# Performance work log

Hardware: AMD Instinct MI355X
Metric: run time of the kernel (lower is better)

Reference implementation:

```python
import jax, jax.numpy as jnp
import numpy as np

S, B, D, K, E = 2048, 16, 256, 2048, 1048576  # seq_len, batch, input_dim, max_seq_len, n_edges


def setup_inputs() -> dict:
    key = jax.random.key(0)
    k1, k2, k3, k4, k5 = jax.random.split(key, 5)
    M = jax.random.normal(k1, (S, B, D), dtype=jnp.float32)
    W = jax.random.normal(k2, (K, D), dtype=jnp.float32) * (1.0 / np.sqrt(D))
    lengths = jax.random.randint(k3, (B,), 1, S, dtype=jnp.int64)
    edge_batch = jax.random.randint(k4, (E,), 0, B, dtype=jnp.int64)
    edge_ij = jax.random.randint(k5, (E, 2), 0, K, dtype=jnp.int64)
    return {"M": M, "W": W, "lengths": lengths, "edge_batch": edge_batch, "edge_ij": edge_ij}


def reference(M, W, lengths, edge_batch, edge_ij):
    # scale = Linear(input_dim, max_seq_len, bias=False): (S, B, K)
    scale = jnp.einsum('sbd,kd->sbk', M, W)
    # softmax over the sequence dim (dim=0), then permute(1,2,0) -> (B, K, S)
    alpha = jnp.transpose(jax.nn.softmax(scale, axis=0), (1, 2, 0))
    # mask = ones*1e-10 with edges set to 1; mask_copy = zeros with edges set to 1
    mask = jnp.full(alpha.shape, 1e-10, dtype=alpha.dtype)
    mask = mask.at[edge_batch, edge_ij[:, 0], edge_ij[:, 1]].set(1.0)
    mask_copy = jnp.zeros(alpha.shape, dtype=alpha.dtype)
    mask_copy = mask_copy.at[edge_batch, edge_ij[:, 0], edge_ij[:, 1]].set(1.0)
    masked_alpha = alpha * mask
    sums = masked_alpha.sum(-1, keepdims=True)
    scores = (masked_alpha / sums) * mask_copy
    return scores
```

## Files before the change

kernel.cpp:

```cpp
#include <hip/hip_runtime.h>

#define S_LEN 2048
#define B_DIM 16
#define D_DIM 256
#define K_DIM 2048
#define E_NUM 1048576

typedef __attribute__((ext_vector_type(4))) float f32x4;
typedef __attribute__((ext_vector_type(8))) short s16x8;
typedef __attribute__((ext_vector_type(4))) unsigned short u16x4;

__device__ __forceinline__ unsigned short f2bf(float f) {
    unsigned int u = __float_as_uint(f);
    u += 0x7fffu + ((u >> 16) & 1u);
    return (unsigned short)(u >> 16);
}

__global__ void prep_kernel(const float* __restrict__ W, const float* __restrict__ M,
                            unsigned short* __restrict__ Wbf, unsigned short* __restrict__ Mbf,
                            unsigned long long* __restrict__ mw) {
    int bid = blockIdx.x;
    if (bid < 2048) {
        int t = bid * 256 + threadIdx.x;
        ((f32x4*)mw)[t] = (f32x4){0.f, 0.f, 0.f, 0.f};
    } else if (bid < 2560) {
        int t = (bid - 2048) * 256 + threadIdx.x;
        f32x4 v = ((const f32x4*)W)[t];
        u16x4 u;
        u.x = f2bf(v.x); u.y = f2bf(v.y); u.z = f2bf(v.z); u.w = f2bf(v.w);
        ((u16x4*)Wbf)[t] = u;
    } else {
        int t = (bid - 2560) * 256 + threadIdx.x;
        f32x4 v = ((const f32x4*)M)[t];
        int flat4 = t * 4;
        int d0 = flat4 & 255;
        int sb = flat4 >> 8;
        int b  = sb & 15;
        int s  = sb >> 4;
        u16x4 u;
        u.x = f2bf(v.x); u.y = f2bf(v.y); u.z = f2bf(v.z); u.w = f2bf(v.w);
        *(u16x4*)&Mbf[((size_t)(b * S_LEN + s)) * D_DIM + d0] = u;
    }
}

__global__ void maskbuild_kernel(const int* __restrict__ eb, const int* __restrict__ ij,
                                 unsigned long long* __restrict__ mw) {
    int e = blockIdx.x * 256 + threadIdx.x;
    int b = eb[e];
    int2 p = *(const int2*)&ij[2 * e];
    size_t w = ((size_t)(b * K_DIM + p.x)) * 32 + (p.y >> 6);
    atomicOr(&mw[w], 1ull << (p.y & 63));
}

__launch_bounds__(256, 2)
__global__ void gemm6_kernel(const unsigned short* __restrict__ Mbf,
                             const unsigned short* __restrict__ Wbf,
                             const unsigned long long* __restrict__ mw,
                             float* __restrict__ out) {
    __shared__ unsigned short Msh[64 * 256];
    __shared__ float sc[64 * 128];
    __shared__ float smZ[4][2][16];
    __shared__ float smE[4][2][16];

    const int tid  = threadIdx.x;
    const int x    = blockIdx.x;
    const int b    = ((x & 7) << 1) | ((x >> 3) & 1);
    const int k0   = (x >> 4) * 64;
    const int lane = tid & 63;
    const int w    = tid >> 6;
    const int wk   = w & 1;
    const int ws   = w >> 1;
    const int r    = lane & 15;
    const int g    = lane >> 4;

    const unsigned short* MB = Mbf + (size_t)b * S_LEN * D_DIM;
    const int kc0 = k0 + wk * 32 + r;
    const size_t mrow0 = (size_t)(b * K_DIM + kc0) * 32;

    s16x8 breg[2][8];
    #pragma unroll
    for (int ks = 0; ks < 2; ++ks)
        #pragma unroll
        for (int d = 0; d < 8; ++d)
            breg[ks][d] = *(const s16x8*)&Wbf[(size_t)(kc0 + ks * 16) * D_DIM + d * 32 + g * 8];

    const int lrh  = lane >> 5;
    const int lc16 = lane & 31;

    auto stage = [&](int bufi, int t) {
        const int s0 = t * 64;
        unsigned short* buf = bufi ? (unsigned short*)sc : Msh;
        #pragma unroll
        for (int c = 0; c < 8; ++c) {
            const int row   = w * 16 + c * 2 + lrh;
            const int col16 = lc16 ^ (row & 7);
            const unsigned short* src = MB + (size_t)(s0 + row) * D_DIM + col16 * 8;
            char* dst = (char*)buf + w * 8192 + c * 1024;
            __builtin_amdgcn_global_load_lds(
                (__attribute__((address_space(1))) const void*)src,
                (__attribute__((address_space(3))) void*)dst, 16, 0, 0);
        }
    };

    float Zl[2]  = {0.f, 0.f};
    float Zel[2] = {0.f, 0.f};

    stage(0, 0);
    __syncthreads();

    for (int t = 0; t < 32; ++t) {
        if (t < 31) stage((t & 1) ^ 1, t + 1);
        const unsigned long long wv0 = mw[mrow0 + t];
        const unsigned long long wv1 = mw[mrow0 + 512 + t];
        const unsigned short* cur = (t & 1) ? (const unsigned short*)sc : Msh;

        f32x4 acc[2][2];
        #pragma unroll
        for (int q = 0; q < 2; ++q)
            #pragma unroll
            for (int ks = 0; ks < 2; ++ks) acc[q][ks] = (f32x4){0.f, 0.f, 0.f, 0.f};

        #pragma unroll
        for (int d = 0; d < 8; ++d) {
            const int acol = ((d * 4 + g) ^ (r & 7)) * 8;
            #pragma unroll
            for (int q = 0; q < 2; ++q) {
                s16x8 a = *(const s16x8*)&cur[(ws * 32 + q * 16 + r) * 256 + acol];
                acc[q][0] = __builtin_amdgcn_mfma_f32_16x16x32_bf16(a, breg[0][d], acc[q][0], 0, 0, 0);
                acc[q][1] = __builtin_amdgcn_mfma_f32_16x16x32_bf16(a, breg[1][d], acc[q][1], 0, 0, 0);
            }
        }

        #pragma unroll
        for (int q = 0; q < 2; ++q) {
            const int sh = ws * 32 + q * 16 + g * 4;
            #pragma unroll
            for (int rr = 0; rr < 4; ++rr) {
                float e0 = __expf(acc[q][0][rr]);
                float e1 = __expf(acc[q][1][rr]);
                Zl[0] += e0; Zl[1] += e1;
                Zel[0] += ((wv0 >> (sh + rr)) & 1ull) ? e0 : 0.f;
                Zel[1] += ((wv1 >> (sh + rr)) & 1ull) ? e1 : 0.f;
            }
        }
        __syncthreads();
    }

    stage(0, 0);

    #pragma unroll
    for (int ks = 0; ks < 2; ++ks) {
        Zl[ks]  += __shfl_xor(Zl[ks], 16);  Zl[ks]  += __shfl_xor(Zl[ks], 32);
        Zel[ks] += __shfl_xor(Zel[ks], 16); Zel[ks] += __shfl_xor(Zel[ks], 32);
    }
    if (g == 0) {
        smZ[w][0][r] = Zl[0]; smZ[w][1][r] = Zl[1];
        smE[w][0][r] = Zel[0]; smE[w][1][r] = Zel[1];
    }
    __syncthreads();
    float rdv[2];
    #pragma unroll
    for (int ks = 0; ks < 2; ++ks) {
        float Z  = Zl[ks]  + smZ[w ^ 2][ks][r];
        float Ze = Zel[ks] + smE[w ^ 2][ks][r];
        rdv[ks] = 1.0f / (1e-10f * (Z - Ze) + Ze);
    }

    for (int t = 0; t < 32; ++t) {
        const int h = t & 1;
        const unsigned long long wv0 = mw[mrow0 + t];
        const unsigned long long wv1 = mw[mrow0 + 512 + t];

        f32x4 acc[2][2];
        #pragma unroll
        for (int q = 0; q < 2; ++q)
            #pragma unroll
            for (int ks = 0; ks < 2; ++ks) acc[q][ks] = (f32x4){0.f, 0.f, 0.f, 0.f};

        #pragma unroll
        for (int d = 0; d < 8; ++d) {
            const int acol = ((d * 4 + g) ^ (r & 7)) * 8;
            #pragma unroll
            for (int q = 0; q < 2; ++q) {
                s16x8 a = *(const s16x8*)&Msh[(ws * 32 + q * 16 + r) * 256 + acol];
                acc[q][0] = __builtin_amdgcn_mfma_f32_16x16x32_bf16(a, breg[0][d], acc[q][0], 0, 0, 0);
                acc[q][1] = __builtin_amdgcn_mfma_f32_16x16x32_bf16(a, breg[1][d], acc[q][1], 0, 0, 0);
            }
        }

        #pragma unroll
        for (int q = 0; q < 2; ++q) {
            const int sh = ws * 32 + q * 16 + g * 4;
            #pragma unroll
            for (int ks = 0; ks < 2; ++ks) {
                const unsigned long long bits = ks ? wv1 : wv0;
                const int row = wk * 32 + ks * 16 + r;
                const int colb = h * 64 + ws * 32 + q * 16 + g * 4;
                const int phys = ((colb >> 2) ^ (row & 31));
                f32x4 v;
                #pragma unroll
                for (int rr = 0; rr < 4; ++rr) {
                    bool edge = (bits >> (sh + rr)) & 1ull;
                    v[rr] = edge ? __expf(acc[q][ks][rr]) * rdv[ks] : 0.f;
                }
                *(f32x4*)&sc[row * 128 + phys * 4] = v;
            }
        }
        __syncthreads();

        if (t < 31) stage(0, t + 1);
        if (h) {
            const int sg = t >> 1;
            const int slot = lane & 31;
            #pragma unroll
            for (int i = 0; i < 8; ++i) {
                const int row = w * 16 + i * 2 + lrh;
                f32x4 v = *(const f32x4*)&sc[row * 128 + (slot ^ (row & 31)) * 4];
                *(f32x4*)&out[(size_t)(b * K_DIM + k0 + row) * S_LEN + sg * 128 + slot * 4] = v;
            }
        }
        if (t < 31) __syncthreads();
    }
}

extern "C" void kernel_launch(void* const* d_in, const int* in_sizes, int n_in,
                              void* d_out, int out_size, void* d_ws, size_t ws_size,
                              hipStream_t stream) {
    (void)in_sizes; (void)n_in; (void)ws_size; (void)out_size;
    const float* M  = (const float*)d_in[0];
    const float* W  = (const float*)d_in[1];
    const int* eb   = (const int*)d_in[3];
    const int* ij   = (const int*)d_in[4];
    float* out      = (float*)d_out;
    char* ws        = (char*)d_ws;

    unsigned long long* mw = (unsigned long long*)ws;
    unsigned short* Wbf = (unsigned short*)(ws + 8388608);
    unsigned short* Mbf = (unsigned short*)(ws + 9437184);

    prep_kernel<<<10752, 256, 0, stream>>>(W, M, Wbf, Mbf, mw);
    maskbuild_kernel<<<E_NUM / 256, 256, 0, stream>>>(eb, ij, mw);
    gemm6_kernel<<<512, 256, 0, stream>>>(Mbf, Wbf, mw, out);
}
```

Measured before the change: 176.4 us.

## Store raw masked logits in first pass and fix up edges sparsely

Removes the second GEMM pass that recomputed the logits. The first pass now writes masked raw logits (zero off-edge) directly to the output with nontemporal stores. After the row normalisers are reduced, a sparse sweep over the edge bitmask reads back only the edge entries and overwrites them with exp(x)*rdv. This halves the MFMA work and drops the LDS transpose buffer, at the cost of scattered read-modify-write traffic on about 3% of the output and dense stores that are no longer staged through LDS.

```diff
diff --git a/kernel.cpp b/kernel.cpp
--- a/kernel.cpp
+++ b/kernel.cpp
@@ -53,14 +53,14 @@
 }
 
 __launch_bounds__(256, 2)
-__global__ void gemm6_kernel(const unsigned short* __restrict__ Mbf,
+__global__ void gemm7_kernel(const unsigned short* __restrict__ Mbf,
                              const unsigned short* __restrict__ Wbf,
                              const unsigned long long* __restrict__ mw,
                              float* __restrict__ out) {
-    __shared__ unsigned short Msh[64 * 256];
-    __shared__ float sc[64 * 128];
+    __shared__ unsigned short Msh[2][64 * 256];
     __shared__ float smZ[4][2][16];
     __shared__ float smE[4][2][16];
+    __shared__ float sm_rd[64];
 
     const int tid  = threadIdx.x;
     const int x    = blockIdx.x;
@@ -89,7 +89,7 @@
 
     auto stage = [&](int bufi, int t) {
         const int s0 = t * 64;
-        unsigned short* buf = bufi ? (unsigned short*)sc : Msh;
+        unsigned short* buf = &Msh[bufi][0];
         #pragma unroll
         for (int c = 0; c < 8; ++c) {
             const int row   = w * 16 + c * 2 + lrh;
@@ -112,7 +112,7 @@
         if (t < 31) stage((t & 1) ^ 1, t + 1);
         const unsigned long long wv0 = mw[mrow0 + t];
         const unsigned long long wv1 = mw[mrow0 + 512 + t];
-        const unsigned short* cur = (t & 1) ? (const unsigned short*)sc : Msh;
+        const unsigned short* cur = &Msh[t & 1][0];
 
         f32x4 acc[2][2];
         #pragma unroll
@@ -135,18 +135,25 @@
         for (int q = 0; q < 2; ++q) {
             const int sh = ws * 32 + q * 16 + g * 4;
             #pragma unroll
-            for (int rr = 0; rr < 4; ++rr) {
-                float e0 = __expf(acc[q][0][rr]);
-                float e1 = __expf(acc[q][1][rr]);
-                Zl[0] += e0; Zl[1] += e1;
-                Zel[0] += ((wv0 >> (sh + rr)) & 1ull) ? e0 : 0.f;
-                Zel[1] += ((wv1 >> (sh + rr)) & 1ull) ? e1 : 0.f;
+            for (int ks = 0; ks < 2; ++ks) {
+                const unsigned long long bits = ks ? wv1 : wv0;
+                f32x4 ov;
+                #pragma unroll
+                for (int rr = 0; rr < 4; ++rr) {
+                    float v = acc[q][ks][rr];
+                    float e = __expf(v);
+                    Zl[ks] += e;
+                    bool edge = (bits >> (sh + rr)) & 1ull;
+                    Zel[ks] += edge ? e : 0.f;
+                    ov[rr] = edge ? v : 0.f;
+                }
+                __builtin_nontemporal_store(ov,
+                    (f32x4*)&out[(size_t)(b * K_DIM + kc0 + ks * 16) * S_LEN
+                                 + t * 64 + ws * 32 + q * 16 + g * 4]);
             }
         }
         __syncthreads();
     }
-
-    stage(0, 0);
 
     #pragma unroll
     for (int ks = 0; ks < 2; ++ks) {
@@ -158,68 +165,29 @@
         smE[w][0][r] = Zel[0]; smE[w][1][r] = Zel[1];
     }
     __syncthreads();
-    float rdv[2];
     #pragma unroll
     for (int ks = 0; ks < 2; ++ks) {
         float Z  = Zl[ks]  + smZ[w ^ 2][ks][r];
         float Ze = Zel[ks] + smE[w ^ 2][ks][r];
-        rdv[ks] = 1.0f / (1e-10f * (Z - Ze) + Ze);
-    }
-
-    for (int t = 0; t < 32; ++t) {
-        const int h = t & 1;
-        const unsigned long long wv0 = mw[mrow0 + t];
-        const unsigned long long wv1 = mw[mrow0 + 512 + t];
-
-        f32x4 acc[2][2];
-        #pragma unroll
-        for (int q = 0; q < 2; ++q)
-            #pragma unroll
-            for (int ks = 0; ks < 2; ++ks) acc[q][ks] = (f32x4){0.f, 0.f, 0.f, 0.f};
-
-        #pragma unroll
-        for (int d = 0; d < 8; ++d) {
-            const int acol = ((d * 4 + g) ^ (r & 7)) * 8;
-            #pragma unroll
-            for (int q = 0; q < 2; ++q) {
-                s16x8 a = *(const s16x8*)&Msh[(ws * 32 + q * 16 + r) * 256 + acol];
-                acc[q][0] = __builtin_amdgcn_mfma_f32_16x16x32_bf16(a, breg[0][d], acc[q][0], 0, 0, 0);
-                acc[q][1] = __builtin_amdgcn_mfma_f32_16x16x32_bf16(a, breg[1][d], acc[q][1], 0, 0, 0);
-            }
-        }
-
-        #pragma unroll
-        for (int q = 0; q < 2; ++q) {
-            const int sh = ws * 32 + q * 16 + g * 4;
-            #pragma unroll
-            for (int ks = 0; ks < 2; ++ks) {
-                const unsigned long long bits = ks ? wv1 : wv0;
-                const int row = wk * 32 + ks * 16 + r;
-                const int colb = h * 64 + ws * 32 + q * 16 + g * 4;
-                const int phys = ((colb >> 2) ^ (row & 31));
-                f32x4 v;
-                #pragma unroll
-                for (int rr = 0; rr < 4; ++rr) {
-                    bool edge = (bits >> (sh + rr)) & 1ull;
-                    v[rr] = edge ? __expf(acc[q][ks][rr]) * rdv[ks] : 0.f;
-                }
-                *(f32x4*)&sc[row * 128 + phys * 4] = v;
-            }
-        }
-        __syncthreads();
-
-        if (t < 31) stage(0, t + 1);
-        if (h) {
-            const int sg = t >> 1;
-            const int slot = lane & 31;
-            #pragma unroll
-            for (int i = 0; i < 8; ++i) {
-                const int row = w * 16 + i * 2 + lrh;
-                f32x4 v = *(const f32x4*)&sc[row * 128 + (slot ^ (row & 31)) * 4];
-                *(f32x4*)&out[(size_t)(b * K_DIM + k0 + row) * S_LEN + sg * 128 + slot * 4] = v;
-            }
-        }
-        if (t < 31) __syncthreads();
+        float rdv = 1.0f / (1e-10f * (Z - Ze) + Ze);
+        if (ws == 0 && g == 0) sm_rd[wk * 32 + ks * 16 + r] = rdv;
+    }
+    __threadfence();
+    __syncthreads();
+
+    for (int it = tid; it < 64 * 32; it += 256) {
+        const int kl = it >> 5;
+        const int wj = it & 31;
+        unsigned long long bits = mw[(size_t)(b * K_DIM + k0 + kl) * 32 + wj];
+        if (!bits) continue;
+        const float rdrow = sm_rd[kl];
+        const size_t rowo = (size_t)(b * K_DIM + k0 + kl) * S_LEN + wj * 64;
+        while (bits) {
+            const int j = __builtin_ctzll(bits);
+            bits &= bits - 1;
+            const float xv = out[rowo + j];
+            out[rowo + j] = __expf(xv) * rdrow;
+        }
     }
 }
 
@@ -240,5 +208,5 @@
 
     prep_kernel<<<10752, 256, 0, stream>>>(W, M, Wbf, Mbf, mw);
     maskbuild_kernel<<<E_NUM / 256, 256, 0, stream>>>(eb, ij, mw);
-    gemm6_kernel<<<512, 256, 0, stream>>>(Mbf, Wbf, mw, out);
-}
+    gemm7_kernel<<<512, 256, 0, stream>>>(Mbf, Wbf, mw, out);
+}
```

Result: slower. 277.1 us (+57.1%).

## Replace two-pass GEMM softmax with single pass plus sparse finalize kernel

Applied to the files above, without the earlier changes.

The GEMM kernel previously ran the full bf16 MFMA product twice, once to accumulate softmax denominators and once to write normalized outputs. It now runs a single pass that writes raw logits at edge positions (zeros elsewhere), accumulates the sums, and stores per-row reciprocals to a workspace buffer. A new finalize kernel walks the mask bitmap and rewrites only the edge entries as exp(logit)*reciprocal. This halves the matmul work in exchange for an extra launch and a scattered read-modify-write of about a million output elements.

```diff
diff --git a/kernel.cpp b/kernel.cpp
--- a/kernel.cpp
+++ b/kernel.cpp
@@ -53,9 +53,10 @@
 }
 
 __launch_bounds__(256, 2)
-__global__ void gemm6_kernel(const unsigned short* __restrict__ Mbf,
+__global__ void gemm9_kernel(const unsigned short* __restrict__ Mbf,
                              const unsigned short* __restrict__ Wbf,
                              const unsigned long long* __restrict__ mw,
+                             float* __restrict__ rd,
                              float* __restrict__ out) {
     __shared__ unsigned short Msh[64 * 256];
     __shared__ float sc[64 * 128];
@@ -87,15 +88,14 @@
     const int lrh  = lane >> 5;
     const int lc16 = lane & 31;
 
-    auto stage = [&](int bufi, int t) {
+    auto stage = [&](int t) {
         const int s0 = t * 64;
-        unsigned short* buf = bufi ? (unsigned short*)sc : Msh;
         #pragma unroll
         for (int c = 0; c < 8; ++c) {
             const int row   = w * 16 + c * 2 + lrh;
             const int col16 = lc16 ^ (row & 7);
             const unsigned short* src = MB + (size_t)(s0 + row) * D_DIM + col16 * 8;
-            char* dst = (char*)buf + w * 8192 + c * 1024;
+            char* dst = (char*)Msh + w * 8192 + c * 1024;
             __builtin_amdgcn_global_load_lds(
                 (__attribute__((address_space(1))) const void*)src,
                 (__attribute__((address_space(3))) void*)dst, 16, 0, 0);
@@ -105,66 +105,8 @@
     float Zl[2]  = {0.f, 0.f};
     float Zel[2] = {0.f, 0.f};
 
-    stage(0, 0);
+    stage(0);
     __syncthreads();
-
-    for (int t = 0; t < 32; ++t) {
-        if (t < 31) stage((t & 1) ^ 1, t + 1);
-        const unsigned long long wv0 = mw[mrow0 + t];
-        const unsigned long long wv1 = mw[mrow0 + 512 + t];
-        const unsigned short* cur = (t & 1) ? (const unsigned short*)sc : Msh;
-
-        f32x4 acc[2][2];
-        #pragma unroll
-        for (int q = 0; q < 2; ++q)
-            #pragma unroll
-            for (int ks = 0; ks < 2; ++ks) acc[q][ks] = (f32x4){0.f, 0.f, 0.f, 0.f};
-
-        #pragma unroll
-        for (int d = 0; d < 8; ++d) {
-            const int acol = ((d * 4 + g) ^ (r & 7)) * 8;
-            #pragma unroll
-            for (int q = 0; q < 2; ++q) {
-                s16x8 a = *(const s16x8*)&cur[(ws * 32 + q * 16 + r) * 256 + acol];
-                acc[q][0] = __builtin_amdgcn_mfma_f32_16x16x32_bf16(a, breg[0][d], acc[q][0], 0, 0, 0);
-                acc[q][1] = __builtin_amdgcn_mfma_f32_16x16x32_bf16(a, breg[1][d], acc[q][1], 0, 0, 0);
-            }
-        }
-
-        #pragma unroll
-        for (int q = 0; q < 2; ++q) {
-            const int sh = ws * 32 + q * 16 + g * 4;
-            #pragma unroll
-            for (int rr = 0; rr < 4; ++rr) {
-                float e0 = __expf(acc[q][0][rr]);
-                float e1 = __expf(acc[q][1][rr]);
-                Zl[0] += e0; Zl[1] += e1;
-                Zel[0] += ((wv0 >> (sh + rr)) & 1ull) ? e0 : 0.f;
-                Zel[1] += ((wv1 >> (sh + rr)) & 1ull) ? e1 : 0.f;
-            }
-        }
-        __syncthreads();
-    }
-
-    stage(0, 0);
-
-    #pragma unroll
-    for (int ks = 0; ks < 2; ++ks) {
-        Zl[ks]  += __shfl_xor(Zl[ks], 16);  Zl[ks]  += __shfl_xor(Zl[ks], 32);
-        Zel[ks] += __shfl_xor(Zel[ks], 16); Zel[ks] += __shfl_xor(Zel[ks], 32);
-    }
-    if (g == 0) {
-        smZ[w][0][r] = Zl[0]; smZ[w][1][r] = Zl[1];
-        smE[w][0][r] = Zel[0]; smE[w][1][r] = Zel[1];
-    }
-    __syncthreads();
-    float rdv[2];
-    #pragma unroll
-    for (int ks = 0; ks < 2; ++ks) {
-        float Z  = Zl[ks]  + smZ[w ^ 2][ks][r];
-        float Ze = Zel[ks] + smE[w ^ 2][ks][r];
-        rdv[ks] = 1.0f / (1e-10f * (Z - Ze) + Ze);
-    }
 
     for (int t = 0; t < 32; ++t) {
         const int h = t & 1;
@@ -200,15 +142,19 @@
                 f32x4 v;
                 #pragma unroll
                 for (int rr = 0; rr < 4; ++rr) {
+                    float xv = acc[q][ks][rr];
+                    float e = __expf(xv);
+                    Zl[ks] += e;
                     bool edge = (bits >> (sh + rr)) & 1ull;
-                    v[rr] = edge ? __expf(acc[q][ks][rr]) * rdv[ks] : 0.f;
+                    Zel[ks] += edge ? e : 0.f;
+                    v[rr] = edge ? xv : 0.f;
                 }
                 *(f32x4*)&sc[row * 128 + phys * 4] = v;
             }
         }
         __syncthreads();
 
-        if (t < 31) stage(0, t + 1);
+        if (t < 31) stage(t + 1);
         if (h) {
             const int sg = t >> 1;
             const int slot = lane & 31;
@@ -220,6 +166,42 @@
             }
         }
         if (t < 31) __syncthreads();
+    }
+
+    #pragma unroll
+    for (int ks = 0; ks < 2; ++ks) {
+        Zl[ks]  += __shfl_xor(Zl[ks], 16);  Zl[ks]  += __shfl_xor(Zl[ks], 32);
+        Zel[ks] += __shfl_xor(Zel[ks], 16); Zel[ks] += __shfl_xor(Zel[ks], 32);
+    }
+    if (g == 0) {
+        smZ[w][0][r] = Zl[0]; smZ[w][1][r] = Zl[1];
+        smE[w][0][r] = Zel[0]; smE[w][1][r] = Zel[1];
+    }
+    __syncthreads();
+    if (ws == 0 && g == 0) {
+        #pragma unroll
+        for (int ks = 0; ks < 2; ++ks) {
+            float Z  = smZ[w][ks][r] + smZ[w ^ 2][ks][r];
+            float Ze = smE[w][ks][r] + smE[w ^ 2][ks][r];
+            rd[b * K_DIM + k0 + wk * 32 + ks * 16 + r] =
+                1.0f / (1e-10f * (Z - Ze) + Ze);
+        }
+    }
+}
+
+__global__ void finalize_kernel(const unsigned long long* __restrict__ mw,
+                                const float* __restrict__ rd,
+                                float* __restrict__ out) {
+    int t = blockIdx.x * 256 + threadIdx.x;
+    unsigned long long bits = mw[t];
+    if (!bits) return;
+    const int row = t >> 5;
+    const float rdv = rd[row];
+    const size_t base = (size_t)row * S_LEN + (t & 31) * 64;
+    while (bits) {
+        const int j = __builtin_ctzll(bits);
+        bits &= bits - 1;
+        out[base + j] = __expf(out[base + j]) * rdv;
     }
 }
 
@@ -237,8 +219,10 @@
     unsigned long long* mw = (unsigned long long*)ws;
     unsigned short* Wbf = (unsigned short*)(ws + 8388608);
     unsigned short* Mbf = (unsigned short*)(ws + 9437184);
+    float* rd = (float*)(ws + 26214400);
 
     prep_kernel<<<10752, 256, 0, stream>>>(W, M, Wbf, Mbf, mw);
     maskbuild_kernel<<<E_NUM / 256, 256, 0, stream>>>(eb, ij, mw);
-    gemm6_kernel<<<512, 256, 0, stream>>>(Mbf, Wbf, mw, out);
-}
+    gemm9_kernel<<<512, 256, 0, stream>>>(Mbf, Wbf, mw, rd, out);
+    finalize_kernel<<<4096, 256, 0, stream>>>(mw, rd, out);
+}
```

Result: no change. 173.6 us (median of 3 runs) (-1.6%).
